# Kernel tuning notes

Hardware: AMD Instinct MI355X
Metric: run time of the kernel (lower is better)

Reference implementation:

```python
import jax, jax.numpy as jnp
import numpy as np

B, N, D, H = 8, 2048, 128, 8
HD = D // H  # head_depth = 16
CLIP = 10.0
INF = 1e10
THETA = 10000.0
SCALE_BASE = 512.0
LOGIT_SCALE = float(np.log(400.0) / np.log(50.0) / np.sqrt(HD))


def _rotate_half(x):
    # interleaved pairs: (x1, x2) -> (-x2, x1)
    x1 = x[..., ::2]
    x2 = x[..., 1::2]
    return jnp.stack((-x2, x1), axis=-1).reshape(x.shape)


def _rope_xpos(n, hd):
    # rotary_embedding_torch RotaryEmbedding(dim=hd, use_xpos=True)
    inv_freq = 1.0 / (THETA ** (jnp.arange(0, hd, 2, dtype=jnp.float32) / hd))  # (hd/2,)
    t = jnp.arange(n, dtype=jnp.float32)
    freqs = t[:, None] * inv_freq[None, :]          # (n, hd/2)
    freqs = jnp.repeat(freqs, 2, axis=-1)           # (n, hd) interleaved dup
    sc = (jnp.arange(0, hd, 2, dtype=jnp.float32) + 0.4 * hd) / (1.4 * hd)  # (hd/2,)
    power = (t - (n // 2)) / SCALE_BASE             # centered positions
    scale = sc[None, :] ** power[:, None]           # (n, hd/2)
    scale = jnp.repeat(scale, 2, axis=-1)           # (n, hd)
    return freqs, scale


def setup_inputs() -> dict:
    key = jax.random.key(0)
    ks = jax.random.split(key, 7)
    stdv_qkv = 1.0 / np.sqrt(HD)
    stdv_out = 1.0 / np.sqrt(D)
    q = jax.random.normal(ks[0], (B, N, D), dtype=jnp.float32)
    k = jax.random.normal(ks[1], (B, N, D), dtype=jnp.float32)
    v = jax.random.normal(ks[2], (B, N, D), dtype=jnp.float32)
    Wq = jax.random.uniform(ks[3], (D, D), minval=-stdv_qkv, maxval=stdv_qkv, dtype=jnp.float32)
    Wk = jax.random.uniform(ks[4], (D, D), minval=-stdv_qkv, maxval=stdv_qkv, dtype=jnp.float32)
    Wv = jax.random.uniform(ks[5], (D, D), minval=-stdv_qkv, maxval=stdv_qkv, dtype=jnp.float32)
    Wout = jax.random.uniform(ks[6], (D, D), minval=-stdv_out, maxval=stdv_out, dtype=jnp.float32)
    mask = jnp.zeros((B, N, 1), dtype=bool)
    return {"q": q, "k": k, "v": v, "Wq": Wq, "Wk": Wk, "Wv": Wv, "Wout": Wout, "mask": mask}


def reference(q, k, v, Wq, Wk, Wv, Wout, mask):
    def split_heads(t, W):
        # torch Linear (bias=False): t @ W.T, then (B,N,H,HD) -> (B,H,N,HD)
        return (t @ W.T).reshape(B, N, H, HD).transpose(0, 2, 1, 3)

    Qh = split_heads(q, Wq)
    Kh = split_heads(k, Wk)
    Vh = split_heads(v, Wv)

    freqs, scale = _rope_xpos(N, HD)  # (N, HD) each, broadcast over (B,H,N,HD)
    cos, sin = jnp.cos(freqs), jnp.sin(freqs)
    Qr = Qh * (cos * scale) + _rotate_half(Qh) * (sin * scale)
    inv_scale = 1.0 / scale
    Kr = Kh * (cos * inv_scale) + _rotate_half(Kh) * (sin * inv_scale)

    logits = jnp.einsum('bhqd,bhkd->bhqk', Qr, Kr) * LOGIT_SCALE
    logits = CLIP * jnp.tanh(logits)
    # mask: (B,N,1) bool, True -> masked; broadcast to (B,1,1,N)
    logits = jnp.where(mask[:, None, None, :, 0], -INF, logits)
    probs = jax.nn.softmax(logits, axis=-1)
    out = jnp.einsum('bhqk,bhkd->bhqd', probs, Vh)
    out = out.transpose(0, 2, 1, 3).reshape(B, N, D)
    return out @ Wout.T
```

## Files before the change

kernel.cpp:

```cpp
#include <hip/hip_runtime.h>
#include <math.h>

#define BB 8
#define NN 2048
#define DD 128
#define HH 8

typedef _Float16 v4h __attribute__((ext_vector_type(4)));
typedef float    v4f __attribute__((ext_vector_type(4)));

__device__ __forceinline__ v4f zero4() { v4f z = {0.f, 0.f, 0.f, 0.f}; return z; }

__device__ __forceinline__ v4f mfma16(v4h a, v4h b, v4f c) {
    return __builtin_amdgcn_mfma_f32_16x16x16f16(a, b, c, 0, 0, 0);
}

__device__ __forceinline__ float fexp2(float x) {
#if __has_builtin(__builtin_amdgcn_exp2f)
    return __builtin_amdgcn_exp2f(x);
#else
    return __expf(x * 0.69314718055994531f);
#endif
}

#define QSCALE 1.10478088f
#define C1F 14.426950408889634f
#define C2F 28.853900817779268f

__global__ __launch_bounds__(256) void prep_kernel(
    const float* __restrict__ Wq, const float* __restrict__ Wk,
    const float* __restrict__ Wv, const float* __restrict__ Wo,
    _Float16* __restrict__ WH, _Float16* __restrict__ WoH,
    float* __restrict__ rtab)
{
    int tid = blockIdx.x * 256 + threadIdx.x;
    int m = tid >> 14, i = tid & 16383;
    const float* src = (m == 0) ? Wq : (m == 1) ? Wk : (m == 2) ? Wv : Wo;
    float wv = src[i];
    if (m < 3) WH[m * 16384 + i] = (_Float16)wv;
    else       WoH[i] = (_Float16)wv;

    if (tid < NN * 16) {
        int t = tid >> 4, hd = tid & 15, j = hd >> 1;
        const float invf_tab[8] = {1.f, 0.31622776601683794f, 0.1f, 0.031622776601683791f,
                                   0.01f, 0.0031622776601683794f, 0.001f, 0.00031622776601683794f};
        float freq = (float)t * invf_tab[j];
        float c = cosf(freq), s = sinf(freq);
        float scf = ((float)(2 * j) + 6.4f) / 22.4f;
        float pw  = ((float)t - 1024.0f) / 512.0f;
        float scl = exp2f(pw * log2f(scf));
        rtab[0 * NN * 16 + tid] = c * scl * QSCALE;
        rtab[1 * NN * 16 + tid] = s * scl * QSCALE;
        float is = 1.0f / scl;
        rtab[2 * NN * 16 + tid] = c * is;
        rtab[3 * NN * 16 + tid] = s * is;
    }
}

__global__ __launch_bounds__(256) void proj_rope_kernel(
    const float* __restrict__ q, const float* __restrict__ k, const float* __restrict__ v,
    const _Float16* __restrict__ WH, const float* __restrict__ rtab,
    _Float16* __restrict__ Qr, _Float16* __restrict__ Kr, _Float16* __restrict__ VT)
{
    __shared__ __align__(16) _Float16 xb[64][136];
    const int tid = threadIdx.x;
    const int m  = blockIdx.y;
    const int r0 = blockIdx.x * 64;
    const int b  = r0 >> 11;
    const int n0 = r0 & 2047;

    const float* s = ((m == 0) ? q : (m == 1) ? k : v) + (size_t)r0 * 128;
    #pragma unroll
    for (int i = 0; i < 8; ++i) {
        int u = tid + i * 256;
        int row = u >> 5, c4 = (u & 31) * 4;
        v4f f = *(const v4f*)(s + row * 128 + c4);
        v4h hv; hv[0]=(_Float16)f[0]; hv[1]=(_Float16)f[1]; hv[2]=(_Float16)f[2]; hv[3]=(_Float16)f[3];
        *(v4h*)&xb[row][c4] = hv;
    }
    __syncthreads();

    const int w = tid >> 6, lane = tid & 63;
    const int l16 = lane & 15, quad = lane >> 4;

    v4h xf[8];
    #pragma unroll
    for (int kt = 0; kt < 8; ++kt)
        xf[kt] = *(const v4h*)&xb[w * 16 + l16][kt * 16 + quad * 4];
    const _Float16* Wm = WH + m * 16384;
    v4f acc[8];
    #pragma unroll
    for (int ct = 0; ct < 8; ++ct) acc[ct] = zero4();
    #pragma unroll
    for (int kt = 0; kt < 8; ++kt) {
        #pragma unroll
        for (int ct = 0; ct < 8; ++ct) {
            v4h wf = *(const v4h*)(Wm + (ct * 16 + l16) * 128 + kt * 16 + quad * 4);
            if (m < 2) acc[ct] = mfma16(wf, xf[kt], acc[ct]);
            else       acc[ct] = mfma16(xf[kt], wf, acc[ct]);
        }
    }
    if (m < 2) {
        const float* tc = rtab + (m == 0 ? 0 : 2 * NN * 16);
        const float* ts = tc + NN * 16;
        const int n = n0 + w * 16 + l16;
        _Float16* dst = (m == 0 ? Qr : Kr);
        #pragma unroll
        for (int ct = 0; ct < 8; ++ct) {
            v4f cs = *(const v4f*)(tc + n * 16 + quad * 4);
            v4f sn = *(const v4f*)(ts + n * 16 + quad * 4);
            v4f a = acc[ct];
            v4f rot; rot[0] = -a[1]; rot[1] = a[0]; rot[2] = -a[3]; rot[3] = a[2];
            v4h o;
            #pragma unroll
            for (int r = 0; r < 4; ++r) o[r] = (_Float16)(a[r] * cs[r] + rot[r] * sn[r]);
            *(v4h*)(dst + ((size_t)(b * 8 + ct) * NN + n) * 16 + quad * 4) = o;
        }
    } else {
        #pragma unroll
        for (int ct = 0; ct < 8; ++ct) {
            v4f a = acc[ct];
            v4h o;
            #pragma unroll
            for (int r = 0; r < 4; ++r) o[r] = (_Float16)a[r];
            *(v4h*)(VT + ((size_t)(b * 8 + ct) * 16 + l16) * NN + n0 + w * 16 + quad * 4) = o;
        }
    }
}

__global__ __launch_bounds__(512, 8) void attn_kernel(
    const _Float16* __restrict__ Qr, const _Float16* __restrict__ Kr,
    const _Float16* __restrict__ VT, const unsigned char* __restrict__ mask,
    _Float16* __restrict__ Obuf)
{
    __shared__ __align__(16) _Float16 Kt[128][20];
    __shared__ __align__(16) _Float16 VTt[16][136];
    __shared__ __align__(16) float    av[128];

    const int tid = threadIdx.x;
    const int bh = blockIdx.x >> 4;
    const int qt = blockIdx.x & 15;
    const int b = bh >> 3, h = bh & 7;
    const int q0 = qt * 128;
    const int w = tid >> 6, lane = tid & 63;
    const int l16 = lane & 15, quad = lane >> 4;

    const int qrow = q0 + w * 16 + l16;
    v4h qf = *(const v4h*)(Qr + ((size_t)bh * NN + qrow) * 16 + quad * 4);

    v4f ot = zero4();
    v4f sa = zero4();
    v4h ones; ones[0] = ones[1] = ones[2] = ones[3] = (_Float16)1.f;

    const int srow = tid >> 2, sc4 = (tid & 3) * 4;
    const int vhd = tid >> 5, vn4 = (tid & 31) * 4;

    for (int k0 = 0; k0 < NN; k0 += 128) {
        __syncthreads();
        *(v4h*)&Kt[srow][sc4]  = *(const v4h*)(Kr + ((size_t)bh * NN + k0 + srow) * 16 + sc4);
        *(v4h*)&VTt[vhd][vn4]  = *(const v4h*)(VT + ((size_t)bh * 16 + vhd) * NN + k0 + vn4);
        if (tid < 128) av[tid] = mask[b * NN + k0 + tid] ? -1e30f : C1F;
        __syncthreads();

        #pragma unroll
        for (int st = 0; st < 8; ++st) {
            v4h kf = *(const v4h*)&Kt[st * 16 + l16][quad * 4];
            v4f ad = *(const v4f*)&av[st * 16 + quad * 4];
            v4h vf = *(const v4h*)&VTt[l16][st * 16 + quad * 4];
            v4f sv = mfma16(kf, qf, zero4());
            v4h ph;
            #pragma unroll
            for (int r = 0; r < 4; ++r) {
                float u  = fexp2(sv[r]);
                float rc = __builtin_amdgcn_rcpf(u + 1.f);
                float p  = fexp2(__builtin_fmaf(rc, -C2F, ad[r]));
                ph[r] = (_Float16)p;
            }
            ot = mfma16(vf, ph, ot);
            sa = mfma16(ones, ph, sa);
        }
    }
    float rd = 1.0f / sa[0];
    v4h o;
    #pragma unroll
    for (int r = 0; r < 4; ++r) o[r] = (_Float16)(ot[r] * rd);
    *(v4h*)(Obuf + ((size_t)(b * NN + qrow) * 128) + h * 16 + quad * 4) = o;
}

__global__ __launch_bounds__(256) void outproj_kernel(
    const _Float16* __restrict__ Obuf, const _Float16* __restrict__ WoH,
    float* __restrict__ out)
{
    __shared__ __align__(16) _Float16 ob[64][136];
    const int tid = threadIdx.x;
    const int r0 = blockIdx.x * 64;
    const int ct0 = blockIdx.y * 2;
    #pragma unroll
    for (int i = 0; i < 8; ++i) {
        int u = tid + i * 256;
        int row = u >> 5, c4 = (u & 31) * 4;
        *(v4h*)&ob[row][c4] = *(const v4h*)(Obuf + (size_t)(r0 + row) * 128 + c4);
    }
    __syncthreads();
    const int w = tid >> 6, lane = tid & 63;
    const int l16 = lane & 15, quad = lane >> 4;
    v4h af[8];
    #pragma unroll
    for (int kt = 0; kt < 8; ++kt)
        af[kt] = *(const v4h*)&ob[w * 16 + l16][kt * 16 + quad * 4];
    v4f acc[2];
    #pragma unroll
    for (int c = 0; c < 2; ++c) acc[c] = zero4();
    #pragma unroll
    for (int kt = 0; kt < 8; ++kt)
        #pragma unroll
        for (int c = 0; c < 2; ++c) {
            v4h wf = *(const v4h*)(WoH + ((ct0 + c) * 16 + l16) * 128 + kt * 16 + quad * 4);
            acc[c] = mfma16(af[kt], wf, acc[c]);
        }
    #pragma unroll
    for (int c = 0; c < 2; ++c)
        #pragma unroll
        for (int r = 0; r < 4; ++r)
            out[(size_t)(r0 + w * 16 + quad * 4 + r) * 128 + (ct0 + c) * 16 + l16] = acc[c][r];
}

extern "C" void kernel_launch(void* const* d_in, const int* in_sizes, int n_in,
                              void* d_out, int out_size, void* d_ws, size_t ws_size,
                              hipStream_t stream)
{
    const float* q  = (const float*)d_in[0];
    const float* k  = (const float*)d_in[1];
    const float* v  = (const float*)d_in[2];
    const float* Wq = (const float*)d_in[3];
    const float* Wk = (const float*)d_in[4];
    const float* Wv = (const float*)d_in[5];
    const float* Wo = (const float*)d_in[6];
    const unsigned char* mask = (const unsigned char*)d_in[7];
    float* out = (float*)d_out;

    char* ws = (char*)d_ws;
    _Float16* WH   = (_Float16*)(ws);
    _Float16* WoH  = (_Float16*)(ws + 98304);
    float*    rtab = (float*)(ws + 131072);
    _Float16* Qr   = (_Float16*)(ws + 655360);
    _Float16* Kr   = (_Float16*)(ws + 4849664);
    _Float16* VTd  = (_Float16*)(ws + 9043968);
    _Float16* Obuf = (_Float16*)(ws + 13238272);

    prep_kernel<<<256, 256, 0, stream>>>(Wq, Wk, Wv, Wo, WH, WoH, rtab);
    proj_rope_kernel<<<dim3(256, 3), 256, 0, stream>>>(q, k, v, WH, rtab, Qr, Kr, VTd);
    attn_kernel<<<1024, 512, 0, stream>>>(Qr, Kr, VTd, mask, Obuf);
    outproj_kernel<<<dim3(256, 4), 256, 0, stream>>>(Obuf, WoH, out);
}
```

Baseline: 196.4 us.

## Switch attention to 32x32x16 MFMA tiles with 4 waves per block

New measurement: 196.0 us. No clear change (-0.2%).

```diff
diff --git a/kernel.cpp b/kernel.cpp
--- a/kernel.cpp
+++ b/kernel.cpp
@@ -7,12 +7,23 @@
 #define HH 8
 
 typedef _Float16 v4h __attribute__((ext_vector_type(4)));
+typedef _Float16 v8h __attribute__((ext_vector_type(8)));
 typedef float    v4f __attribute__((ext_vector_type(4)));
+typedef float    v16f __attribute__((ext_vector_type(16)));
 
 __device__ __forceinline__ v4f zero4() { v4f z = {0.f, 0.f, 0.f, 0.f}; return z; }
+__device__ __forceinline__ v16f zero16() {
+    v16f z;
+    #pragma unroll
+    for (int i = 0; i < 16; ++i) z[i] = 0.f;
+    return z;
+}
 
 __device__ __forceinline__ v4f mfma16(v4h a, v4h b, v4f c) {
     return __builtin_amdgcn_mfma_f32_16x16x16f16(a, b, c, 0, 0, 0);
+}
+__device__ __forceinline__ v16f mfma32(v8h a, v8h b, v16f c) {
+    return __builtin_amdgcn_mfma_f32_32x32x16_f16(a, b, c, 0, 0, 0);
 }
 
 __device__ __forceinline__ float fexp2(float x) {
@@ -128,14 +139,15 @@
     }
 }
 
-__global__ __launch_bounds__(512, 8) void attn_kernel(
+__global__ __launch_bounds__(256, 6) void attn_kernel(
     const _Float16* __restrict__ Qr, const _Float16* __restrict__ Kr,
     const _Float16* __restrict__ VT, const unsigned char* __restrict__ mask,
     _Float16* __restrict__ Obuf)
 {
-    __shared__ __align__(16) _Float16 Kt[128][20];
-    __shared__ __align__(16) _Float16 VTt[16][136];
-    __shared__ __align__(16) float    av[128];
+    __shared__ __align__(16) char smem[15360];
+    _Float16* Kt = (_Float16*)smem;
+    _Float16* Ve = (_Float16*)(smem + 6144);
+    float*    av = (float*)(smem + 14848);
 
     const int tid = threadIdx.x;
     const int bh = blockIdx.x >> 4;
@@ -143,48 +155,85 @@
     const int b = bh >> 3, h = bh & 7;
     const int q0 = qt * 128;
     const int w = tid >> 6, lane = tid & 63;
-    const int l16 = lane & 15, quad = lane >> 4;
-
-    const int qrow = q0 + w * 16 + l16;
-    v4h qf = *(const v4h*)(Qr + ((size_t)bh * NN + qrow) * 16 + quad * 4);
-
-    v4f ot = zero4();
-    v4f sa = zero4();
-    v4h ones; ones[0] = ones[1] = ones[2] = ones[3] = (_Float16)1.f;
-
-    const int srow = tid >> 2, sc4 = (tid & 3) * 4;
-    const int vhd = tid >> 5, vn4 = (tid & 31) * 4;
+    const int l32 = lane & 31, hi = lane >> 5;
+
+    const int qrow = q0 + w * 32 + l32;
+    v8h qf = *(const v8h*)(Qr + ((size_t)bh * NN + qrow) * 16 + hi * 8);
+
+    {
+        v8h one8;
+        #pragma unroll
+        for (int i = 0; i < 8; ++i) one8[i] = (_Float16)1.f;
+        *(v8h*)(Ve + (16 + (tid >> 4)) * 136 + (tid & 15) * 8) = one8;
+    }
+
+    v16f acc = zero16();
+
+    const int krow = tid >> 1, kpar = tid & 1;
+    const int vhd = tid >> 4, vg = tid & 15;
 
     for (int k0 = 0; k0 < NN; k0 += 128) {
         __syncthreads();
-        *(v4h*)&Kt[srow][sc4]  = *(const v4h*)(Kr + ((size_t)bh * NN + k0 + srow) * 16 + sc4);
-        *(v4h*)&VTt[vhd][vn4]  = *(const v4h*)(VT + ((size_t)bh * 16 + vhd) * NN + k0 + vn4);
+        v8h kv = *(const v8h*)(Kr + ((size_t)bh * NN + k0 + krow) * 16 + kpar * 8);
+        *(v8h*)(Kt + krow * 24 + kpar * 8) = kv;
+        v8h vv = *(const v8h*)(VT + ((size_t)bh * 16 + vhd) * NN + k0 + vg * 8);
+        {
+            _Float16* vb = Ve + vhd * 136 + (vg >> 1) * 16 + (vg & 1) * 4;
+            v4h lo4, hi4;
+            lo4[0]=vv[0]; lo4[1]=vv[1]; lo4[2]=vv[2]; lo4[3]=vv[3];
+            hi4[0]=vv[4]; hi4[1]=vv[5]; hi4[2]=vv[6]; hi4[3]=vv[7];
+            *(v4h*)(vb)     = lo4;
+            *(v4h*)(vb + 8) = hi4;
+        }
         if (tid < 128) av[tid] = mask[b * NN + k0 + tid] ? -1e30f : C1F;
         __syncthreads();
 
         #pragma unroll
-        for (int st = 0; st < 8; ++st) {
-            v4h kf = *(const v4h*)&Kt[st * 16 + l16][quad * 4];
-            v4f ad = *(const v4f*)&av[st * 16 + quad * 4];
-            v4h vf = *(const v4h*)&VTt[l16][st * 16 + quad * 4];
-            v4f sv = mfma16(kf, qf, zero4());
-            v4h ph;
-            #pragma unroll
-            for (int r = 0; r < 4; ++r) {
+        for (int kc = 0; kc < 4; ++kc) {
+            v8h kf = *(const v8h*)(Kt + (kc * 32 + l32) * 24 + hi * 8);
+            v16f sv = mfma32(kf, qf, zero16());
+
+            v4f ad[4];
+            #pragma unroll
+            for (int g = 0; g < 4; ++g)
+                ad[g] = *(const v4f*)(av + kc * 32 + g * 8 + hi * 4);
+
+            float p[16];
+            #pragma unroll
+            for (int r = 0; r < 16; ++r) {
                 float u  = fexp2(sv[r]);
                 float rc = __builtin_amdgcn_rcpf(u + 1.f);
-                float p  = fexp2(__builtin_fmaf(rc, -C2F, ad[r]));
-                ph[r] = (_Float16)p;
+                p[r] = fexp2(__builtin_fmaf(rc, -C2F, ad[r >> 2][r & 3]));
             }
-            ot = mfma16(vf, ph, ot);
-            sa = mfma16(ones, ph, sa);
-        }
-    }
-    float rd = 1.0f / sa[0];
-    v4h o;
-    #pragma unroll
-    for (int r = 0; r < 4; ++r) o[r] = (_Float16)(ot[r] * rd);
-    *(v4h*)(Obuf + ((size_t)(b * NN + qrow) * 128) + h * 16 + quad * 4) = o;
+
+            #pragma unroll
+            for (int c2 = 0; c2 < 2; ++c2) {
+                v8h pa;
+                #pragma unroll
+                for (int j = 0; j < 8; ++j) pa[j] = (_Float16)p[c2 * 8 + j];
+                v8h vf = *(const v8h*)(Ve + l32 * 136 + (kc * 2 + c2) * 16 + hi * 8);
+                acc = mfma32(pa, vf, acc);
+            }
+        }
+    }
+
+    float rs[16];
+    #pragma unroll
+    for (int r = 0; r < 16; ++r) rs[r] = __shfl_xor(acc[r], 16, 64);
+
+    __syncthreads();
+    _Float16* myOt = (_Float16*)smem + w * 768;
+    if (!(lane & 16)) {
+        int j = lane & 15;
+        #pragma unroll
+        for (int r = 0; r < 16; ++r) {
+            int qr = (r & 3) + 8 * (r >> 2) + 4 * hi;
+            myOt[qr * 24 + j] = (_Float16)(acc[r] * __builtin_amdgcn_rcpf(rs[r]));
+        }
+    }
+    asm volatile("s_waitcnt lgkmcnt(0)" ::: "memory");
+    v8h ov = *(const v8h*)(myOt + (lane >> 1) * 24 + (lane & 1) * 8);
+    *(v8h*)(Obuf + ((size_t)(b * NN + q0 + w * 32 + (lane >> 1)) * 128) + h * 16 + (lane & 1) * 8) = ov;
 }
 
 __global__ __launch_bounds__(256) void outproj_kernel(
@@ -250,6 +299,6 @@
 
     prep_kernel<<<256, 256, 0, stream>>>(Wq, Wk, Wv, Wo, WH, WoH, rtab);
     proj_rope_kernel<<<dim3(256, 3), 256, 0, stream>>>(q, k, v, WH, rtab, Qr, Kr, VTd);
-    attn_kernel<<<1024, 512, 0, stream>>>(Qr, Kr, VTd, mask, Obuf);
+    attn_kernel<<<1024, 256, 0, stream>>>(Qr, Kr, VTd, mask, Obuf);
     outproj_kernel<<<dim3(256, 4), 256, 0, stream>>>(Obuf, WoH, out);
 }
```
